# Optimization experiments

Measured on AMD Instinct MI355X. Metric: run time of the kernel, lower is better.

The kernel has to match this reference:

```python
import jax, jax.numpy as jnp
import numpy as np

B, S, H, E, I, TOPK = 4, 1024, 1024, 8, 2048, 2
SOFT_CAP = 30.0
W_SCALE = 0.02


def setup_inputs() -> dict:
    key = jax.random.key(0)
    k0, k1, k2, k3, k4 = jax.random.split(key, 5)
    return {
        "hidden_states": jax.random.normal(k0, (B, S, H), dtype=jnp.float32),
        "w_gate": jax.random.normal(k1, (E, H), dtype=jnp.float32) * W_SCALE,
        "w1": jax.random.normal(k2, (E, I, H), dtype=jnp.float32) * W_SCALE,
        "w3": jax.random.normal(k3, (E, I, H), dtype=jnp.float32) * W_SCALE,
        "w2": jax.random.normal(k4, (E, H, I), dtype=jnp.float32) * W_SCALE,
        "top_k": TOPK,
    }


def reference(hidden_states, w_gate, w1, w3, w2, top_k):
    orig_shape = hidden_states.shape
    x = hidden_states.reshape(-1, orig_shape[-1])  # [T, H]
    # Router gate + soft cap
    logits = x @ w_gate.T  # [T, E]
    logits = SOFT_CAP * jnp.tanh(logits / SOFT_CAP)
    probs = jax.nn.softmax(logits, axis=-1)
    # top-k routing, renormalize=False -> use softmax probs directly
    top_w, top_i = jax.lax.top_k(probs, top_k)  # [T, k]
    T, nE = probs.shape
    gates = jnp.zeros((T, nE), probs.dtype).at[
        jnp.arange(T)[:, None], top_i
    ].add(top_w)  # [T, E] sparse routing weights
    # Grouped expert GEMMs with gated GELU (GeluAndMul)
    h1 = jnp.einsum('th,eih->tei', x, w1)  # [T, E, I]
    h3 = jnp.einsum('th,eih->tei', x, w3)
    act = jax.nn.gelu(h1, approximate=False) * h3
    y = jnp.einsum('tei,ehi->teh', act, w2)  # [T, E, H]
    out = jnp.einsum('te,teh->th', gates, y)
    return out.reshape(orig_shape)
```

## Files before the change

kernel.cpp:

```cpp
#include <hip/hip_runtime.h>
#include <stdint.h>

#define T_TOK 4096
#define HDIM  1024
#define NEXP  8
#define IDIM  2048
#define BK    64
#define NASSIGN (T_TOK * 2)

typedef short short8 __attribute__((ext_vector_type(8)));
typedef float f32x4 __attribute__((ext_vector_type(4)));

__device__ __forceinline__ unsigned short f32_to_bf16(float f) {
  union { float f; uint32_t u; } v; v.f = f;
  uint32_t r = 0x7FFFu + ((v.u >> 16) & 1u);
  return (unsigned short)((v.u + r) >> 16);
}

__device__ __forceinline__ void gload16(const void* g, void* l) {
  __builtin_amdgcn_global_load_lds(
      (const __attribute__((address_space(1))) uint32_t*)g,
      (__attribute__((address_space(3))) uint32_t*)l, 16, 0, 0);
}

__global__ void cast_w3_kernel(const float* __restrict__ w1,
                               const float* __restrict__ w3,
                               const float* __restrict__ w2,
                               unsigned short* __restrict__ w1b,
                               unsigned short* __restrict__ w3b,
                               unsigned short* __restrict__ w2b, int n8) {
  int i = blockIdx.x * blockDim.x + threadIdx.x;
  if (i >= n8) return;
  const float* src; unsigned short* dst;
  if (blockIdx.y == 0)      { src = w1; dst = w1b; }
  else if (blockIdx.y == 1) { src = w3; dst = w3b; }
  else                      { src = w2; dst = w2b; }
  const float4* s = (const float4*)src + (size_t)i * 2;
  float4 a = s[0], b = s[1];
  short8 o;
  o[0] = f32_to_bf16(a.x); o[1] = f32_to_bf16(a.y);
  o[2] = f32_to_bf16(a.z); o[3] = f32_to_bf16(a.w);
  o[4] = f32_to_bf16(b.x); o[5] = f32_to_bf16(b.y);
  o[6] = f32_to_bf16(b.z); o[7] = f32_to_bf16(b.w);
  ((short8*)dst)[i] = o;
}

__global__ __launch_bounds__(256)
void router_core(const float* __restrict__ x, const float* __restrict__ wg,
                 unsigned short* __restrict__ xb,
                 unsigned char* __restrict__ eids,
                 float* __restrict__ gate_a) {
  __shared__ float wgs[NEXP * HDIM];
  const int tid = threadIdx.x;
#pragma unroll
  for (int i = 0; i < NEXP * HDIM / 4 / 256; ++i)
    ((float4*)wgs)[i * 256 + tid] = ((const float4*)wg)[i * 256 + tid];
  __syncthreads();

  const int wv = tid >> 6, lane = tid & 63;
#pragma unroll
  for (int tt = 0; tt < 2; ++tt) {
    const int t = blockIdx.x * 8 + wv * 2 + tt;
    const float* xr = x + (size_t)t * HDIM;
    float acc0 = 0.f, acc1v = 0.f, acc2 = 0.f, acc3 = 0.f;
    float acc4 = 0.f, acc5 = 0.f, acc6 = 0.f, acc7 = 0.f;
#pragma unroll
    for (int it = 0; it < 4; ++it) {
      const int j = it * 256 + lane * 4;
      const float4 xv = *(const float4*)(xr + j);
      ushort4 u;
      u.x = f32_to_bf16(xv.x); u.y = f32_to_bf16(xv.y);
      u.z = f32_to_bf16(xv.z); u.w = f32_to_bf16(xv.w);
      *(ushort4*)(xb + (size_t)t * HDIM + j) = u;
      const float4 g0 = *(const float4*)(wgs + 0 * HDIM + j);
      const float4 g1 = *(const float4*)(wgs + 1 * HDIM + j);
      const float4 g2 = *(const float4*)(wgs + 2 * HDIM + j);
      const float4 g3 = *(const float4*)(wgs + 3 * HDIM + j);
      const float4 g4 = *(const float4*)(wgs + 4 * HDIM + j);
      const float4 g5 = *(const float4*)(wgs + 5 * HDIM + j);
      const float4 g6 = *(const float4*)(wgs + 6 * HDIM + j);
      const float4 g7 = *(const float4*)(wgs + 7 * HDIM + j);
      acc0 += xv.x * g0.x + xv.y * g0.y + xv.z * g0.z + xv.w * g0.w;
      acc1v += xv.x * g1.x + xv.y * g1.y + xv.z * g1.z + xv.w * g1.w;
      acc2 += xv.x * g2.x + xv.y * g2.y + xv.z * g2.z + xv.w * g2.w;
      acc3 += xv.x * g3.x + xv.y * g3.y + xv.z * g3.z + xv.w * g3.w;
      acc4 += xv.x * g4.x + xv.y * g4.y + xv.z * g4.z + xv.w * g4.w;
      acc5 += xv.x * g5.x + xv.y * g5.y + xv.z * g5.z + xv.w * g5.w;
      acc6 += xv.x * g6.x + xv.y * g6.y + xv.z * g6.z + xv.w * g6.w;
      acc7 += xv.x * g7.x + xv.y * g7.y + xv.z * g7.z + xv.w * g7.w;
    }
    float acc[NEXP] = {acc0, acc1v, acc2, acc3, acc4, acc5, acc6, acc7};
#pragma unroll
    for (int e = 0; e < NEXP; ++e) {
#pragma unroll
      for (int off = 32; off > 0; off >>= 1) acc[e] += __shfl_xor(acc[e], off);
    }
    if (lane == 0) {
      float p[NEXP];
      float mx = -1e30f;
#pragma unroll
      for (int e = 0; e < NEXP; ++e) {
        float l = 30.0f * tanhf(acc[e] * (1.0f / 30.0f));
        p[e] = l;
        mx = fmaxf(mx, l);
      }
      float s = 0.f;
#pragma unroll
      for (int e = 0; e < NEXP; ++e) { p[e] = expf(p[e] - mx); s += p[e]; }
      const float inv = 1.0f / s;
#pragma unroll
      for (int e = 0; e < NEXP; ++e) p[e] *= inv;
      int i0 = 0;
#pragma unroll
      for (int e = 1; e < NEXP; ++e) if (p[e] > p[i0]) i0 = e;
      int i1 = (i0 == 0) ? 1 : 0;
#pragma unroll
      for (int e = 0; e < NEXP; ++e) if (e != i1 && e != i0 && p[e] > p[i1]) i1 = e;
      eids[t * 2]     = (unsigned char)i0;
      gate_a[t * 2]   = p[i0];
      eids[t * 2 + 1] = (unsigned char)i1;
      gate_a[t * 2 + 1] = p[i1];
    }
  }
}

__global__ __launch_bounds__(1024)
void build_lists(const unsigned char* __restrict__ eids,
                 int* __restrict__ counts, int* __restrict__ list) {
  const int e = blockIdx.x;
  const int tid = threadIdx.x;
  const int wid = tid >> 6, lane = tid & 63;
  __shared__ int wave_tot[16];
  __shared__ int running;
  if (tid == 0) running = 0;
  __syncthreads();
#pragma unroll
  for (int c = 0; c < NASSIGN; c += 1024) {
    const int slot = c + tid;
    const bool match = ((int)eids[slot] == e);
    const unsigned long long mask = __ballot(match);
    if (lane == 0) wave_tot[wid] = __popcll(mask);
    __syncthreads();
    int base = running;
    for (int w = 0; w < wid; ++w) base += wave_tot[w];
    if (match) {
      const int pre = __popcll(mask & ((1ull << lane) - 1ull));
      list[e * T_TOK + base + pre] = slot;
    }
    __syncthreads();
    if (tid == 0) {
      int tot = 0;
      for (int w = 0; w < 16; ++w) tot += wave_tot[w];
      running += tot;
    }
    __syncthreads();
  }
  if (tid == 0) counts[e] = running;
}

__global__ __launch_bounds__(256, 4)
void moe_gemm1_fast(const unsigned short* __restrict__ xb,
                    const unsigned short* __restrict__ w1b,
                    const unsigned short* __restrict__ w3b,
                    const int* __restrict__ counts, const int* __restrict__ list,
                    unsigned short* __restrict__ act) {
  const int e = blockIdx.z;
  const int cnt = counts[e];
  const int m0 = blockIdx.y * 128;
  if (m0 >= cnt) return;
  const int n0 = blockIdx.x * 64;

  __shared__ __align__(16) unsigned short As[128 * BK];
  __shared__ __align__(16) unsigned short B1s[64 * BK];
  __shared__ __align__(16) unsigned short B3s[64 * BK];
  __shared__ int entry_l[128];

  const int tid = threadIdx.x;
  if (tid < 128) entry_l[tid] = (m0 + tid < cnt) ? list[e * T_TOK + m0 + tid] : -1;
  __syncthreads();

  const int lane = tid & 63;
  const int l15 = lane & 15;
  const int kg  = lane >> 4;
  const int wv  = tid >> 6;
  const int wvu = __builtin_amdgcn_readfirstlane(wv);
  const int wm = wv >> 1, wn = wv & 1;

  const int srow8  = lane >> 3;
  const int schunk = (lane & 7) ^ srow8;

  const unsigned short* aSrc[4];
#pragma unroll
  for (int r = 0; r < 4; ++r) {
    const int row = r * 32 + wv * 8 + srow8;
    const int en = entry_l[row];
    const int tok = (en >= 0) ? (en >> 1) : 0;
    aSrc[r] = xb + (size_t)tok * HDIM + schunk * 8;
  }
  const unsigned short* b1Src[2];
  const unsigned short* b3Src[2];
#pragma unroll
  for (int r = 0; r < 2; ++r) {
    const int row = r * 32 + wv * 8 + srow8;
    b1Src[r] = w1b + ((size_t)e * IDIM + n0 + row) * HDIM + schunk * 8;
    b3Src[r] = w3b + ((size_t)e * IDIM + n0 + row) * HDIM + schunk * 8;
  }

  int aOff[4][2], bOff[2][2];
#pragma unroll
  for (int mf = 0; mf < 4; ++mf)
#pragma unroll
    for (int ks = 0; ks < 2; ++ks) {
      const int row = wm * 64 + mf * 16 + l15;
      aOff[mf][ks] = row * 128 + (((ks * 4 + kg) ^ (row & 7)) * 16);
    }
#pragma unroll
  for (int nf = 0; nf < 2; ++nf)
#pragma unroll
    for (int ks = 0; ks < 2; ++ks) {
      const int row = wn * 32 + nf * 16 + l15;
      bOff[nf][ks] = row * 128 + (((ks * 4 + kg) ^ (row & 7)) * 16);
    }

  f32x4 acc1[4][2], acc3[4][2];
#pragma unroll
  for (int mf = 0; mf < 4; ++mf)
#pragma unroll
    for (int nf = 0; nf < 2; ++nf) {
      acc1[mf][nf] = (f32x4){0.f, 0.f, 0.f, 0.f};
      acc3[mf][nf] = (f32x4){0.f, 0.f, 0.f, 0.f};
    }

  const char* AsB = (const char*)As;
  const char* B1B = (const char*)B1s;
  const char* B3B = (const char*)B3s;

  for (int k0 = 0; k0 < HDIM; k0 += BK) {
#pragma unroll
    for (int r = 0; r < 4; ++r) gload16(aSrc[r], As + r * 2048 + wvu * 512);
#pragma unroll
    for (int r = 0; r < 2; ++r) {
      gload16(b1Src[r], B1s + r * 2048 + wvu * 512);
      gload16(b3Src[r], B3s + r * 2048 + wvu * 512);
    }
#pragma unroll
    for (int r = 0; r < 4; ++r) aSrc[r] += BK;
#pragma unroll
    for (int r = 0; r < 2; ++r) { b1Src[r] += BK; b3Src[r] += BK; }
    __syncthreads();

    short8 af[4][2], b1f[2][2], b3f[2][2];
#pragma unroll
    for (int mf = 0; mf < 4; ++mf)
#pragma unroll
      for (int ks = 0; ks < 2; ++ks)
        af[mf][ks] = *(const short8*)(AsB + aOff[mf][ks]);
#pragma unroll
    for (int nf = 0; nf < 2; ++nf)
#pragma unroll
      for (int ks = 0; ks < 2; ++ks) {
        b1f[nf][ks] = *(const short8*)(B1B + bOff[nf][ks]);
        b3f[nf][ks] = *(const short8*)(B3B + bOff[nf][ks]);
      }
#pragma unroll
    for (int mf = 0; mf < 4; ++mf)
#pragma unroll
      for (int nf = 0; nf < 2; ++nf)
#pragma unroll
        for (int ks = 0; ks < 2; ++ks) {
          acc1[mf][nf] = __builtin_amdgcn_mfma_f32_16x16x32_bf16(af[mf][ks], b1f[nf][ks], acc1[mf][nf], 0, 0, 0);
          acc3[mf][nf] = __builtin_amdgcn_mfma_f32_16x16x32_bf16(af[mf][ks], b3f[nf][ks], acc3[mf][nf], 0, 0, 0);
        }
    __syncthreads();
  }

#pragma unroll
  for (int mf = 0; mf < 4; ++mf) {
#pragma unroll
    for (int i = 0; i < 4; ++i) {
      const int r = wm * 64 + mf * 16 + kg * 4 + i;
      const int en = entry_l[r];
      if (en < 0) continue;
      unsigned short* arow = act + (size_t)en * IDIM + n0 + wn * 32;
#pragma unroll
      for (int nf = 0; nf < 2; ++nf) {
        const float h1 = acc1[mf][nf][i];
        const float h3 = acc3[mf][nf][i];
        const float g = 0.5f * h1 * (1.0f + erff(h1 * 0.70710678118f));
        arow[nf * 16 + l15] = f32_to_bf16(g * h3);
      }
    }
  }
}

__global__ __launch_bounds__(512, 2)
void moe_gemm2_fast(const unsigned short* __restrict__ act,
                    const unsigned short* __restrict__ w2b,
                    const int* __restrict__ counts, const int* __restrict__ list,
                    const float* __restrict__ gate_a,
                    float* __restrict__ ybuf) {
  const int e = blockIdx.z;
  const int cnt = counts[e];
  const int m0 = blockIdx.y * 256;
  if (m0 >= cnt) return;
  const int n0 = blockIdx.x * 128;

  __shared__ __align__(16) unsigned short As[256 * BK];
  __shared__ __align__(16) unsigned short Bs[128 * BK];
  __shared__ int entry_l[256];

  const int tid = threadIdx.x;
  if (tid < 256) entry_l[tid] = (m0 + tid < cnt) ? list[e * T_TOK + m0 + tid] : -1;
  __syncthreads();

  const int lane = tid & 63;
  const int l15 = lane & 15;
  const int kg  = lane >> 4;
  const int wid = tid >> 6;
  const int wvu = __builtin_amdgcn_readfirstlane(wid);
  const int wm = wid >> 1, wn = wid & 1;

  const int srow8  = lane >> 3;
  const int schunk = (lane & 7) ^ srow8;

  const unsigned short* aSrc[4];
#pragma unroll
  for (int r = 0; r < 4; ++r) {
    const int row = r * 64 + wid * 8 + srow8;
    const int en = entry_l[row];
    const int arow = (en >= 0) ? en : 0;
    aSrc[r] = act + (size_t)arow * IDIM + schunk * 8;
  }
  const unsigned short* bSrc[2];
#pragma unroll
  for (int r = 0; r < 2; ++r) {
    const int row = r * 64 + wid * 8 + srow8;
    bSrc[r] = w2b + ((size_t)e * HDIM + n0 + row) * IDIM + schunk * 8;
  }

  int aOff[4][2], bOff[4][2];
#pragma unroll
  for (int mf = 0; mf < 4; ++mf)
#pragma unroll
    for (int ks = 0; ks < 2; ++ks) {
      const int row = wm * 64 + mf * 16 + l15;
      aOff[mf][ks] = row * 128 + (((ks * 4 + kg) ^ (row & 7)) * 16);
    }
#pragma unroll
  for (int nf = 0; nf < 4; ++nf)
#pragma unroll
    for (int ks = 0; ks < 2; ++ks) {
      const int row = wn * 64 + nf * 16 + l15;
      bOff[nf][ks] = row * 128 + (((ks * 4 + kg) ^ (row & 7)) * 16);
    }

  f32x4 acc[4][4];
#pragma unroll
  for (int mf = 0; mf < 4; ++mf)
#pragma unroll
    for (int nf = 0; nf < 4; ++nf) acc[mf][nf] = (f32x4){0.f, 0.f, 0.f, 0.f};

  const char* AsB = (const char*)As;
  const char* BsB = (const char*)Bs;

  for (int k0 = 0; k0 < IDIM; k0 += BK) {
#pragma unroll
    for (int r = 0; r < 4; ++r) gload16(aSrc[r], As + r * 4096 + wvu * 512);
#pragma unroll
    for (int r = 0; r < 2; ++r) gload16(bSrc[r], Bs + r * 4096 + wvu * 512);
#pragma unroll
    for (int r = 0; r < 4; ++r) aSrc[r] += BK;
#pragma unroll
    for (int r = 0; r < 2; ++r) bSrc[r] += BK;
    __syncthreads();

    short8 af[4][2], bf[4][2];
#pragma unroll
    for (int mf = 0; mf < 4; ++mf)
#pragma unroll
      for (int ks = 0; ks < 2; ++ks)
        af[mf][ks] = *(const short8*)(AsB + aOff[mf][ks]);
#pragma unroll
    for (int nf = 0; nf < 4; ++nf)
#pragma unroll
      for (int ks = 0; ks < 2; ++ks)
        bf[nf][ks] = *(const short8*)(BsB + bOff[nf][ks]);
#pragma unroll
    for (int mf = 0; mf < 4; ++mf)
#pragma unroll
      for (int nf = 0; nf < 4; ++nf)
#pragma unroll
        for (int ks = 0; ks < 2; ++ks)
          acc[mf][nf] = __builtin_amdgcn_mfma_f32_16x16x32_bf16(af[mf][ks], bf[nf][ks], acc[mf][nf], 0, 0, 0);
    __syncthreads();
  }

#pragma unroll
  for (int mf = 0; mf < 4; ++mf) {
#pragma unroll
    for (int i = 0; i < 4; ++i) {
      const int r = wm * 64 + mf * 16 + kg * 4 + i;
      const int en = entry_l[r];
      if (en < 0) continue;
      const float gate = gate_a[en];
      float* yrow = ybuf + (size_t)en * HDIM + n0 + wn * 64;
#pragma unroll
      for (int nf = 0; nf < 4; ++nf)
        yrow[nf * 16 + l15] = acc[mf][nf][i] * gate;
    }
  }
}

__global__ __launch_bounds__(256)
void combine_kernel(const float* __restrict__ ybuf, float* __restrict__ out) {
  const int i = blockIdx.x * 256 + threadIdx.x;
  const int t  = i >> 8;
  const int j4 = i & 255;
  const float4 a = ((const float4*)(ybuf + (size_t)(2 * t) * HDIM))[j4];
  const float4 b = ((const float4*)(ybuf + (size_t)(2 * t + 1) * HDIM))[j4];
  float4 o;
  o.x = a.x + b.x; o.y = a.y + b.y; o.z = a.z + b.z; o.w = a.w + b.w;
  ((float4*)out)[i] = o;
}

#define LSTRIDE 40

__global__ __launch_bounds__(256, 2)
void moe_gemm1_fb(const unsigned short* __restrict__ xb,
                  const float* __restrict__ w1, const float* __restrict__ w3,
                  const int* __restrict__ counts, const int* __restrict__ list,
                  unsigned short* __restrict__ act) {
  const int e = blockIdx.z;
  const int cnt = counts[e];
  const int m0 = blockIdx.y * 128;
  if (m0 >= cnt) return;
  const int n0 = blockIdx.x * 64;

  __shared__ short As[128 * LSTRIDE];
  __shared__ short B1s[64 * LSTRIDE];
  __shared__ short B3s[64 * LSTRIDE];
  __shared__ int entry_l[128];

  const int tid = threadIdx.x;
  if (tid < 128) entry_l[tid] = (m0 + tid < cnt) ? list[e * T_TOK + m0 + tid] : -1;
  __syncthreads();

  const int lane = tid & 63;
  const int l15 = lane & 15;
  const int kg = lane >> 4;
  const int wv = tid >> 6;
  const int wm = wv >> 1, wn = wv & 1;

  f32x4 acc1[4][2], acc3[4][2];
#pragma unroll
  for (int mf = 0; mf < 4; ++mf)
#pragma unroll
    for (int nf = 0; nf < 2; ++nf) {
      acc1[mf][nf] = (f32x4){0.f, 0.f, 0.f, 0.f};
      acc3[mf][nf] = (f32x4){0.f, 0.f, 0.f, 0.f};
    }

  const int srow = tid >> 2;
  const int scol = (tid & 3) << 3;

  const float* w1base = w1 + ((size_t)e * IDIM + n0) * HDIM;
  const float* w3base = w3 + ((size_t)e * IDIM + n0) * HDIM;

  for (int k0 = 0; k0 < HDIM; k0 += 32) {
#pragma unroll
    for (int it = 0; it < 2; ++it) {
      const int r = srow + it * 64;
      const int en = entry_l[r];
      uint4 v = {0u, 0u, 0u, 0u};
      if (en >= 0)
        v = *(const uint4*)(xb + ((size_t)(en >> 1) * HDIM + k0 + scol));
      *(uint4*)(&As[r * LSTRIDE + scol]) = v;
    }
    {
      const float* p1 = w1base + (size_t)srow * HDIM + k0 + scol;
      float4 a0 = *(const float4*)(p1);
      float4 a1 = *(const float4*)(p1 + 4);
      short8 sb;
      sb[0] = f32_to_bf16(a0.x); sb[1] = f32_to_bf16(a0.y);
      sb[2] = f32_to_bf16(a0.z); sb[3] = f32_to_bf16(a0.w);
      sb[4] = f32_to_bf16(a1.x); sb[5] = f32_to_bf16(a1.y);
      sb[6] = f32_to_bf16(a1.z); sb[7] = f32_to_bf16(a1.w);
      *(short8*)(&B1s[srow * LSTRIDE + scol]) = sb;
      const float* p3 = w3base + (size_t)srow * HDIM + k0 + scol;
      float4 c0 = *(const float4*)(p3);
      float4 c1 = *(const float4*)(p3 + 4);
      sb[0] = f32_to_bf16(c0.x); sb[1] = f32_to_bf16(c0.y);
      sb[2] = f32_to_bf16(c0.z); sb[3] = f32_to_bf16(c0.w);
      sb[4] = f32_to_bf16(c1.x); sb[5] = f32_to_bf16(c1.y);
      sb[6] = f32_to_bf16(c1.z); sb[7] = f32_to_bf16(c1.w);
      *(short8*)(&B3s[srow * LSTRIDE + scol]) = sb;
    }
    __syncthreads();
    short8 af[4], b1f[2], b3f[2];
#pragma unroll
    for (int mf = 0; mf < 4; ++mf)
      af[mf] = *(const short8*)(&As[(wm * 64 + mf * 16 + l15) * LSTRIDE + kg * 8]);
#pragma unroll
    for (int nf = 0; nf < 2; ++nf) {
      b1f[nf] = *(const short8*)(&B1s[(wn * 32 + nf * 16 + l15) * LSTRIDE + kg * 8]);
      b3f[nf] = *(const short8*)(&B3s[(wn * 32 + nf * 16 + l15) * LSTRIDE + kg * 8]);
    }
#pragma unroll
    for (int mf = 0; mf < 4; ++mf)
#pragma unroll
      for (int nf = 0; nf < 2; ++nf) {
        acc1[mf][nf] = __builtin_amdgcn_mfma_f32_16x16x32_bf16(af[mf], b1f[nf], acc1[mf][nf], 0, 0, 0);
        acc3[mf][nf] = __builtin_amdgcn_mfma_f32_16x16x32_bf16(af[mf], b3f[nf], acc3[mf][nf], 0, 0, 0);
      }
    __syncthreads();
  }

#pragma unroll
  for (int mf = 0; mf < 4; ++mf) {
#pragma unroll
    for (int i = 0; i < 4; ++i) {
      const int r = wm * 64 + mf * 16 + kg * 4 + i;
      const int en = entry_l[r];
      if (en < 0) continue;
      unsigned short* arow = act + (size_t)en * IDIM + n0 + wn * 32;
#pragma unroll
      for (int nf = 0; nf < 2; ++nf) {
        const float h1 = acc1[mf][nf][i];
        const float h3 = acc3[mf][nf][i];
        const float g = 0.5f * h1 * (1.0f + erff(h1 * 0.70710678118f));
        arow[nf * 16 + l15] = f32_to_bf16(g * h3);
      }
    }
  }
}

__global__ __launch_bounds__(256, 2)
void moe_gemm2_fb(const unsigned short* __restrict__ act,
                  const float* __restrict__ w2,
                  const int* __restrict__ counts, const int* __restrict__ list,
                  const float* __restrict__ gate_a,
                  float* __restrict__ out) {
  const int e = blockIdx.z;
  const int cnt = counts[e];
  const int m0 = blockIdx.y * 128;
  if (m0 >= cnt) return;
  const int n0 = blockIdx.x * 64;

  __shared__ short As[128 * LSTRIDE];
  __shared__ short Bs[64 * LSTRIDE];
  __shared__ int entry_l[128];

  const int tid = threadIdx.x;
  if (tid < 128) entry_l[tid] = (m0 + tid < cnt) ? list[e * T_TOK + m0 + tid] : -1;
  __syncthreads();

  const int lane = tid & 63;
  const int l15 = lane & 15;
  const int kg = lane >> 4;
  const int wv = tid >> 6;
  const int wm = wv >> 1, wn = wv & 1;

  f32x4 acc[4][2];
#pragma unroll
  for (int mf = 0; mf < 4; ++mf)
#pragma unroll
    for (int nf = 0; nf < 2; ++nf) acc[mf][nf] = (f32x4){0.f, 0.f, 0.f, 0.f};

  const int srow = tid >> 2;
  const int scol = (tid & 3) << 3;

  const float* w2b2 = w2 + ((size_t)e * HDIM + n0) * IDIM;

  for (int k0 = 0; k0 < IDIM; k0 += 32) {
#pragma unroll
    for (int it = 0; it < 2; ++it) {
      const int r = srow + it * 64;
      const int en = entry_l[r];
      uint4 v = {0u, 0u, 0u, 0u};
      if (en >= 0)
        v = *(const uint4*)(act + ((size_t)en * IDIM + k0 + scol));
      *(uint4*)(&As[r * LSTRIDE + scol]) = v;
    }
    {
      const float* p2 = w2b2 + (size_t)srow * IDIM + k0 + scol;
      float4 a0 = *(const float4*)(p2);
      float4 a1 = *(const float4*)(p2 + 4);
      short8 sb;
      sb[0] = f32_to_bf16(a0.x); sb[1] = f32_to_bf16(a0.y);
      sb[2] = f32_to_bf16(a0.z); sb[3] = f32_to_bf16(a0.w);
      sb[4] = f32_to_bf16(a1.x); sb[5] = f32_to_bf16(a1.y);
      sb[6] = f32_to_bf16(a1.z); sb[7] = f32_to_bf16(a1.w);
      *(short8*)(&Bs[srow * LSTRIDE + scol]) = sb;
    }
    __syncthreads();
    short8 af[4], bf[2];
#pragma unroll
    for (int mf = 0; mf < 4; ++mf)
      af[mf] = *(const short8*)(&As[(wm * 64 + mf * 16 + l15) * LSTRIDE + kg * 8]);
#pragma unroll
    for (int nf = 0; nf < 2; ++nf)
      bf[nf] = *(const short8*)(&Bs[(wn * 32 + nf * 16 + l15) * LSTRIDE + kg * 8]);
#pragma unroll
    for (int mf = 0; mf < 4; ++mf)
#pragma unroll
      for (int nf = 0; nf < 2; ++nf)
        acc[mf][nf] = __builtin_amdgcn_mfma_f32_16x16x32_bf16(af[mf], bf[nf], acc[mf][nf], 0, 0, 0);
    __syncthreads();
  }

#pragma unroll
  for (int mf = 0; mf < 4; ++mf) {
#pragma unroll
    for (int i = 0; i < 4; ++i) {
      const int r = wm * 64 + mf * 16 + kg * 4 + i;
      const int en = entry_l[r];
      if (en < 0) continue;
      const float gate = gate_a[en];
      float* orow = out + (size_t)(en >> 1) * HDIM + n0 + wn * 32;
#pragma unroll
      for (int nf = 0; nf < 2; ++nf)
        atomicAdd(&orow[nf * 16 + l15], acc[mf][nf][i] * gate);
    }
  }
}

extern "C" void kernel_launch(void* const* d_in, const int* in_sizes, int n_in,
                              void* d_out, int out_size, void* d_ws, size_t ws_size,
                              hipStream_t stream) {
  const float* x  = (const float*)d_in[0];
  const float* wg = (const float*)d_in[1];
  const float* w1 = (const float*)d_in[2];
  const float* w3 = (const float*)d_in[3];
  const float* w2 = (const float*)d_in[4];
  float* out = (float*)d_out;

  char* ws = (char*)d_ws;
  int*            counts = (int*)ws;
  int*            list   = (int*)(ws + 1024);
  float*          gate_a = (float*)(ws + 132096);
  unsigned char*  eids   = (unsigned char*)(ws + 165888);
  unsigned short* xb     = (unsigned short*)(ws + 262144);
  const size_t OFF_ACT = 262144 + (size_t)T_TOK * HDIM * 2;
  unsigned short* act    = (unsigned short*)(ws + OFF_ACT);
  const size_t WELEMS = (size_t)NEXP * IDIM * HDIM;
  const size_t OFF_W1B = OFF_ACT + (size_t)2 * T_TOK * IDIM * 2;
  const size_t OFF_W3B = OFF_W1B + WELEMS * 2;
  const size_t OFF_W2B = OFF_W3B + WELEMS * 2;
  const size_t WS_NEED = OFF_W2B + WELEMS * 2;

  router_core<<<T_TOK / 8, 256, 0, stream>>>(x, wg, xb, eids, gate_a);
  build_lists<<<NEXP, 1024, 0, stream>>>(eids, counts, list);

  if (ws_size >= WS_NEED) {
    unsigned short* w1b = (unsigned short*)(ws + OFF_W1B);
    unsigned short* w3b = (unsigned short*)(ws + OFF_W3B);
    unsigned short* w2b = (unsigned short*)(ws + OFF_W2B);
    float* ybuf = (float*)(ws + OFF_W1B);
    const int n8 = (int)(WELEMS / 8);
    cast_w3_kernel<<<dim3((n8 + 255) / 256, 3), 256, 0, stream>>>(w1, w3, w2, w1b, w3b, w2b, n8);
    moe_gemm1_fast<<<dim3(IDIM / 64, T_TOK / 128, NEXP), 256, 0, stream>>>(xb, w1b, w3b, counts, list, act);
    moe_gemm2_fast<<<dim3(HDIM / 128, T_TOK / 256, NEXP), 512, 0, stream>>>(act, w2b, counts, list, gate_a, ybuf);
    combine_kernel<<<T_TOK * HDIM / 4 / 256, 256, 0, stream>>>(ybuf, out);
  } else {
    hipMemsetAsync(d_out, 0, (size_t)out_size * sizeof(float), stream);
    moe_gemm1_fb<<<dim3(IDIM / 64, T_TOK / 128, NEXP), 256, 0, stream>>>(xb, w1, w3, counts, list, act);
    moe_gemm2_fb<<<dim3(HDIM / 64, T_TOK / 128, NEXP), 256, 0, stream>>>(act, w2, counts, list, gate_a, out);
  }
}
```

Measured before the change: 227.1 us.

## Fuse weight casts into router and gemm1 launches to overlap work

The w1/w3 fp32-to-bf16 cast moves into extra blocks of the router kernel, and the w2 cast moves into extra blocks of the gemm1 kernel, which now uses a flattened 1D grid. This removes a separate cast launch and lets the memory-bound cast run alongside the router and alongside gemm1 compute. The cost is heavier launches, and the w2 cast blocks compete with gemm1 tiles for bandwidth and CUs. The weight casts still run on every call.

```diff
diff --git a/kernel.cpp b/kernel.cpp
--- a/kernel.cpp
+++ b/kernel.cpp
@@ -7,6 +7,8 @@
 #define IDIM  2048
 #define BK    64
 #define NASSIGN (T_TOK * 2)
+#define N8W   (NEXP * IDIM * HDIM / 8)
+#define CASTBLK (N8W / 256)
 
 typedef short short8 __attribute__((ext_vector_type(8)));
 typedef float f32x4 __attribute__((ext_vector_type(4)));
@@ -23,18 +25,8 @@
       (__attribute__((address_space(3))) uint32_t*)l, 16, 0, 0);
 }
 
-__global__ void cast_w3_kernel(const float* __restrict__ w1,
-                               const float* __restrict__ w3,
-                               const float* __restrict__ w2,
-                               unsigned short* __restrict__ w1b,
-                               unsigned short* __restrict__ w3b,
-                               unsigned short* __restrict__ w2b, int n8) {
-  int i = blockIdx.x * blockDim.x + threadIdx.x;
-  if (i >= n8) return;
-  const float* src; unsigned short* dst;
-  if (blockIdx.y == 0)      { src = w1; dst = w1b; }
-  else if (blockIdx.y == 1) { src = w3; dst = w3b; }
-  else                      { src = w2; dst = w2b; }
+__device__ __forceinline__ void cast8(const float* __restrict__ src,
+                                      unsigned short* __restrict__ dst, int i) {
   const float4* s = (const float4*)src + (size_t)i * 2;
   float4 a = s[0], b = s[1];
   short8 o;
@@ -46,12 +38,24 @@
 }
 
 __global__ __launch_bounds__(256)
-void router_core(const float* __restrict__ x, const float* __restrict__ wg,
+void prep_kernel(const float* __restrict__ x, const float* __restrict__ wg,
                  unsigned short* __restrict__ xb,
                  unsigned char* __restrict__ eids,
-                 float* __restrict__ gate_a) {
+                 float* __restrict__ gate_a,
+                 const float* __restrict__ w1, const float* __restrict__ w3,
+                 unsigned short* __restrict__ w1b, unsigned short* __restrict__ w3b) {
+  const int bid = blockIdx.x;
+  const int tid = threadIdx.x;
+
+  if (bid >= 512) {
+    const int cb = bid - 512;
+    const int i = (cb & (CASTBLK - 1)) * 256 + tid;
+    if (cb < CASTBLK) cast8(w1, w1b, i);
+    else              cast8(w3, w3b, i);
+    return;
+  }
+
   __shared__ float wgs[NEXP * HDIM];
-  const int tid = threadIdx.x;
 #pragma unroll
   for (int i = 0; i < NEXP * HDIM / 4 / 256; ++i)
     ((float4*)wgs)[i * 256 + tid] = ((const float4*)wg)[i * 256 + tid];
@@ -60,7 +64,7 @@
   const int wv = tid >> 6, lane = tid & 63;
 #pragma unroll
   for (int tt = 0; tt < 2; ++tt) {
-    const int t = blockIdx.x * 8 + wv * 2 + tt;
+    const int t = bid * 8 + wv * 2 + tt;
     const float* xr = x + (size_t)t * HDIM;
     float acc0 = 0.f, acc1v = 0.f, acc2 = 0.f, acc3 = 0.f;
     float acc4 = 0.f, acc5 = 0.f, acc6 = 0.f, acc7 = 0.f;
@@ -159,23 +163,32 @@
 }
 
 __global__ __launch_bounds__(256, 4)
-void moe_gemm1_fast(const unsigned short* __restrict__ xb,
-                    const unsigned short* __restrict__ w1b,
-                    const unsigned short* __restrict__ w3b,
-                    const int* __restrict__ counts, const int* __restrict__ list,
-                    unsigned short* __restrict__ act) {
-  const int e = blockIdx.z;
+void gemm1_castw2(const unsigned short* __restrict__ xb,
+                  const unsigned short* __restrict__ w1b,
+                  const unsigned short* __restrict__ w3b,
+                  const int* __restrict__ counts, const int* __restrict__ list,
+                  unsigned short* __restrict__ act,
+                  const float* __restrict__ w2, unsigned short* __restrict__ w2b) {
+  const int bid = blockIdx.x;
+  const int tid = threadIdx.x;
+
+  if (bid >= 8192) {
+    const int i = (bid - 8192) * 256 + tid;
+    cast8(w2, w2b, i);
+    return;
+  }
+
+  const int e  = bid >> 10;
+  const int m0 = ((bid >> 5) & 31) * 128;
+  const int n0 = (bid & 31) * 64;
   const int cnt = counts[e];
-  const int m0 = blockIdx.y * 128;
   if (m0 >= cnt) return;
-  const int n0 = blockIdx.x * 64;
 
   __shared__ __align__(16) unsigned short As[128 * BK];
   __shared__ __align__(16) unsigned short B1s[64 * BK];
   __shared__ __align__(16) unsigned short B3s[64 * BK];
   __shared__ int entry_l[128];
 
-  const int tid = threadIdx.x;
   if (tid < 128) entry_l[tid] = (m0 + tid < cnt) ? list[e * T_TOK + m0 + tid] : -1;
   __syncthreads();
 
@@ -648,20 +661,23 @@
   const size_t OFF_W2B = OFF_W3B + WELEMS * 2;
   const size_t WS_NEED = OFF_W2B + WELEMS * 2;
 
-  router_core<<<T_TOK / 8, 256, 0, stream>>>(x, wg, xb, eids, gate_a);
-  build_lists<<<NEXP, 1024, 0, stream>>>(eids, counts, list);
-
   if (ws_size >= WS_NEED) {
     unsigned short* w1b = (unsigned short*)(ws + OFF_W1B);
     unsigned short* w3b = (unsigned short*)(ws + OFF_W3B);
     unsigned short* w2b = (unsigned short*)(ws + OFF_W2B);
     float* ybuf = (float*)(ws + OFF_W1B);
-    const int n8 = (int)(WELEMS / 8);
-    cast_w3_kernel<<<dim3((n8 + 255) / 256, 3), 256, 0, stream>>>(w1, w3, w2, w1b, w3b, w2b, n8);
-    moe_gemm1_fast<<<dim3(IDIM / 64, T_TOK / 128, NEXP), 256, 0, stream>>>(xb, w1b, w3b, counts, list, act);
+
+    prep_kernel<<<512 + 2 * CASTBLK, 256, 0, stream>>>(x, wg, xb, eids, gate_a,
+                                                       w1, w3, w1b, w3b);
+    build_lists<<<NEXP, 1024, 0, stream>>>(eids, counts, list);
+    gemm1_castw2<<<8192 + CASTBLK, 256, 0, stream>>>(xb, w1b, w3b, counts, list,
+                                                     act, w2, w2b);
     moe_gemm2_fast<<<dim3(HDIM / 128, T_TOK / 256, NEXP), 512, 0, stream>>>(act, w2b, counts, list, gate_a, ybuf);
     combine_kernel<<<T_TOK * HDIM / 4 / 256, 256, 0, stream>>>(ybuf, out);
   } else {
+    prep_kernel<<<512, 256, 0, stream>>>(x, wg, xb, eids, gate_a, w1, w3,
+                                         (unsigned short*)xb, (unsigned short*)xb);
+    build_lists<<<NEXP, 1024, 0, stream>>>(eids, counts, list);
     hipMemsetAsync(d_out, 0, (size_t)out_size * sizeof(float), stream);
     moe_gemm1_fb<<<dim3(IDIM / 64, T_TOK / 128, NEXP), 256, 0, stream>>>(xb, w1, w3, counts, list, act);
     moe_gemm2_fb<<<dim3(HDIM / 64, T_TOK / 128, NEXP), 256, 0, stream>>>(act, w2, counts, list, gate_a, out);
```

New measurement: 212.7 us, median of 3. 1.07x faster.
